# Performance work log

Hardware: AMD Instinct MI355X
Metric: run time of the kernel (lower is better)

## Reference

```python
import jax, jax.numpy as jnp
import numpy as np

NUM_CLASSES = 100000   # vocab (input_dim of the layer)
DIM = 256              # embedding dim (output_dim of the layer)
BATCH = 256
NUM_TRUE = 1024        # hardcoded num_true in call()
NUM_SAMPLED = 16384    # hardcoded num_sampled in call()
LOG_RANGE = float(np.log(NUM_CLASSES + 1.0))


def _sample_log_uniform_unique(rng, n, range_max):
    # Mimics tf log_uniform_candidate_sampler with unique=True: rejection-sample
    # from P(c) ~ log((c+2)/(c+1)) until n unique ids are collected.
    seen = {}
    log_range = np.log(range_max + 1.0)
    while len(seen) < n:
        u = rng.uniform(0.0, log_range, size=2 * n)
        ids = np.minimum(np.floor(np.exp(u) - 1.0).astype(np.int64), range_max - 1)
        for v in ids.tolist():
            if len(seen) >= n:
                break
            seen[v] = None
    return np.fromiter(seen.keys(), dtype=np.int64, count=n)


def setup_inputs() -> dict:
    key = jax.random.key(0)
    k1, k2, k3, k4 = jax.random.split(key, 4)
    inputs = jax.random.normal(k1, (BATCH, DIM), jnp.float32)
    # Original inits w/b to zeros; use small random values for a non-degenerate baseline.
    w = jax.random.normal(k2, (NUM_CLASSES, DIM), jnp.float32) * 0.02
    b = jax.random.normal(k3, (NUM_CLASSES,), jnp.float32) * 0.02
    labels = jax.random.randint(k4, (BATCH, NUM_TRUE), 0, NUM_CLASSES, dtype=jnp.int32)
    rng = np.random.default_rng(0)
    sampled = jnp.asarray(_sample_log_uniform_unique(rng, NUM_SAMPLED, NUM_CLASSES), jnp.int32)
    return {"inputs": inputs, "w": w, "b": b, "labels": labels, "sampled": sampled}


def _log_uniform_prob(ids):
    idf = ids.astype(jnp.float32)
    return jnp.log((idf + 2.0) / (idf + 1.0)) / LOG_RANGE


def _expected_count(ids):
    # P(id appears among NUM_SAMPLED unique candidates) = 1 - (1-p)^NUM_SAMPLED
    p = _log_uniform_prob(ids)
    return -jnp.expm1(NUM_SAMPLED * jnp.log1p(-p))


def _sigmoid_xent(logits, target):
    # numerically stable sigmoid cross-entropy, target is a scalar label value
    return jnp.maximum(logits, 0.0) - logits * target + jnp.log1p(jnp.exp(-jnp.abs(logits)))


def reference(inputs, w, b, labels, sampled):
    # true logits: per-example dot with each true class row  [B, T]
    true_w = w[labels]                                    # [B, T, D] gather
    true_logits = jnp.einsum('bd,btd->bt', inputs, true_w) + b[labels]
    true_logits = true_logits - jnp.log(_expected_count(labels))
    # sampled logits: shared candidate set  [B, S]
    sampled_logits = inputs @ w[sampled].T + b[sampled]
    sampled_logits = sampled_logits - jnp.log(_expected_count(sampled))
    # NCE targets: 1/num_true for true classes, 0 for sampled; sum over columns
    true_xent = _sigmoid_xent(true_logits, 1.0 / NUM_TRUE)
    sampled_xent = _sigmoid_xent(sampled_logits, 0.0)
    return true_xent.sum(axis=1) + sampled_xent.sum(axis=1)   # [B]
```

## Files before the change

### kernel.cpp

```cpp
#include <hip/hip_runtime.h>
#include <hip/hip_bf16.h>

#define NUM_CLASSES 100000
#define DIM 256
#define BATCH 256
#define NUM_TRUE 1024
#define NUM_SAMPLED 16384
#define LOG_RANGE 11.51293546492023f
#define INV_LOG_RANGE (1.0f / LOG_RANGE)

typedef __bf16 bf16x8 __attribute__((ext_vector_type(8)));
typedef float  f32x4  __attribute__((ext_vector_type(4)));

static __device__ __forceinline__ unsigned short f2bf(float f) {
    unsigned int u = __float_as_uint(f);
    unsigned int lsb = (u >> 16) & 1u;
    u += 0x7fffu + lsb;
    return (unsigned short)(u >> 16);
}

static __device__ __forceinline__ float neg_log_ec(int id) {
    float idf = (float)id;
    float p = logf((idf + 2.0f) / (idf + 1.0f)) * INV_LOG_RANGE;
    float ec = -expm1f((float)NUM_SAMPLED * log1pf(-p));
    return -logf(ec);
}

static __device__ __forceinline__ float dot4(float4 a, float4 b) {
    return fmaf(a.x, b.x, fmaf(a.y, b.y, fmaf(a.z, b.z, a.w * b.w)));
}

__global__ __launch_bounds__(256) void comb_kernel(const float* __restrict__ bias,
                                                   float* __restrict__ comb) {
    int c = blockIdx.x * 256 + threadIdx.x;
    if (c < NUM_CLASSES) comb[c] = bias[c] + neg_log_ec(c);
}

__global__ __launch_bounds__(256) void true_kernel(const float* __restrict__ inputs,
                                                   const float* __restrict__ w,
                                                   const float* __restrict__ comb,
                                                   const int* __restrict__ labels,
                                                   float* __restrict__ truep) {
    __shared__ __align__(16) float ins[DIM];
    __shared__ float wsum[4];
    const int tid = threadIdx.x;
    const int b = blockIdx.y;
    ins[tid] = inputs[b * DIM + tid];
    __syncthreads();

    const int lane = tid & 63;
    const int wv   = tid >> 6;
    const int sub  = lane >> 4;
    const int part = lane & 15;
    const float4* ir = (const float4*)ins;
    const float4 in0 = ir[part], in1 = ir[16 + part], in2 = ir[32 + part], in3 = ir[48 + part];

    const int* lab = labels + b * NUM_TRUE + blockIdx.x * 128 + wv * 32;

    float4 buf[2][4];
    float  cb[2];
    #pragma unroll
    for (int s = 0; s < 2; ++s) {
        int l = lab[s * 4 + sub];
        const float4* wr = (const float4*)(w + (size_t)l * DIM);
        buf[s][0] = wr[part];      buf[s][1] = wr[16 + part];
        buf[s][2] = wr[32 + part]; buf[s][3] = wr[48 + part];
        cb[s] = comb[l];
    }

    float acc = 0.0f;
    #pragma unroll
    for (int i = 0; i < 8; ++i) {
        const int cur = i & 1;
        float4 w0 = buf[cur][0], w1 = buf[cur][1], w2 = buf[cur][2], w3 = buf[cur][3];
        float cl = cb[cur];
        if (i < 6) {
            int l = lab[(i + 2) * 4 + sub];
            const float4* wr = (const float4*)(w + (size_t)l * DIM);
            buf[cur][0] = wr[part];      buf[cur][1] = wr[16 + part];
            buf[cur][2] = wr[32 + part]; buf[cur][3] = wr[48 + part];
            cb[cur] = comb[l];
        }
        float d = dot4(w0, in0) + dot4(w1, in1) + dot4(w2, in2) + dot4(w3, in3);
        d += __shfl_xor(d, 1); d += __shfl_xor(d, 2);
        d += __shfl_xor(d, 4); d += __shfl_xor(d, 8);
        float logit = d + cl;
        float v = fmaxf(logit, 0.0f) - logit * (1.0f / (float)NUM_TRUE)
                + __logf(1.0f + __expf(-fabsf(logit)));
        acc += (part == 0) ? v : 0.0f;
    }
    acc += __shfl_xor(acc, 16); acc += __shfl_xor(acc, 32);
    if (lane == 0) wsum[wv] = acc;
    __syncthreads();
    if (tid == 0) truep[b * 8 + blockIdx.x] = wsum[0] + wsum[1] + wsum[2] + wsum[3];
}

#define LWS 264
__global__ __launch_bounds__(256) void sampled_kernel(const float* __restrict__ w,
                                                      const float* __restrict__ comb,
                                                      const int* __restrict__ sampled,
                                                      const float* __restrict__ inputs,
                                                      float* __restrict__ partial) {
    __shared__ unsigned short lw[64][LWS];
    __shared__ unsigned short li[64][LWS];
    __shared__ float cs[64];
    __shared__ float bacc[BATCH];

    const int tid = threadIdx.x;
    const int s0 = blockIdx.x * 64;
    bacc[tid] = 0.0f;

    const int inner = tid & 15;
    const int r16   = tid >> 4;

    #pragma unroll
    for (int rb = 0; rb < 4; ++rb) {
        const int r = rb * 16 + r16;
        const int id = sampled[s0 + r];
        const float* src = w + (size_t)id * DIM;
        #pragma unroll
        for (int j = 0; j < 4; ++j) {
            float4 v = *(const float4*)(src + j * 64 + inner * 4);
            ushort4 pk;
            pk.x = f2bf(v.x); pk.y = f2bf(v.y); pk.z = f2bf(v.z); pk.w = f2bf(v.w);
            *(ushort4*)(&lw[r][j * 64 + inner * 4]) = pk;
        }
    }
    if (tid < 64) cs[tid] = comb[sampled[s0 + tid]];

    const int lane = tid & 63;
    const int wv   = tid >> 6;
    const int m    = lane & 15;
    const int quad = lane >> 4;
    const int wy   = wv & 1;
    const int wx   = wv >> 1;

    for (int chunk = 0; chunk < 4; ++chunk) {
        __syncthreads();
        #pragma unroll
        for (int rb = 0; rb < 4; ++rb) {
            const int r = rb * 16 + r16;
            const float* src = inputs + (size_t)(chunk * 64 + r) * DIM;
            #pragma unroll
            for (int j = 0; j < 4; ++j) {
                float4 v = *(const float4*)(src + j * 64 + inner * 4);
                ushort4 pk;
                pk.x = f2bf(v.x); pk.y = f2bf(v.y); pk.z = f2bf(v.z); pk.w = f2bf(v.w);
                *(ushort4*)(&li[r][j * 64 + inner * 4]) = pk;
            }
        }
        __syncthreads();

        f32x4 acc00 = {0,0,0,0}, acc01 = {0,0,0,0}, acc10 = {0,0,0,0}, acc11 = {0,0,0,0};
        const unsigned short* pa0 = &lw[wy * 32 + m][quad * 8];
        const unsigned short* pa1 = &lw[wy * 32 + 16 + m][quad * 8];
        const unsigned short* pb0 = &li[wx * 32 + m][quad * 8];
        const unsigned short* pb1 = &li[wx * 32 + 16 + m][quad * 8];
        #pragma unroll
        for (int kk = 0; kk < 8; ++kk) {
            bf16x8 a0 = *(const bf16x8*)(pa0 + kk * 32);
            bf16x8 a1 = *(const bf16x8*)(pa1 + kk * 32);
            bf16x8 b0 = *(const bf16x8*)(pb0 + kk * 32);
            bf16x8 b1 = *(const bf16x8*)(pb1 + kk * 32);
            acc00 = __builtin_amdgcn_mfma_f32_16x16x32_bf16(a0, b0, acc00, 0, 0, 0);
            acc01 = __builtin_amdgcn_mfma_f32_16x16x32_bf16(a0, b1, acc01, 0, 0, 0);
            acc10 = __builtin_amdgcn_mfma_f32_16x16x32_bf16(a1, b0, acc10, 0, 0, 0);
            acc11 = __builtin_amdgcn_mfma_f32_16x16x32_bf16(a1, b1, acc11, 0, 0, 0);
        }

        float ps0 = 0.0f, ps1 = 0.0f;
        #pragma unroll
        for (int r = 0; r < 4; ++r) {
            {
                float c = cs[wy * 32 + quad * 4 + r];
                float l0 = acc00[r] + c;
                ps0 += fmaxf(l0, 0.0f) + __logf(1.0f + __expf(-fabsf(l0)));
                float l1 = acc01[r] + c;
                ps1 += fmaxf(l1, 0.0f) + __logf(1.0f + __expf(-fabsf(l1)));
            }
            {
                float c = cs[wy * 32 + 16 + quad * 4 + r];
                float l0 = acc10[r] + c;
                ps0 += fmaxf(l0, 0.0f) + __logf(1.0f + __expf(-fabsf(l0)));
                float l1 = acc11[r] + c;
                ps1 += fmaxf(l1, 0.0f) + __logf(1.0f + __expf(-fabsf(l1)));
            }
        }
        ps0 += __shfl_xor(ps0, 16); ps0 += __shfl_xor(ps0, 32);
        ps1 += __shfl_xor(ps1, 16); ps1 += __shfl_xor(ps1, 32);
        if (quad == 0) {
            atomicAdd(&bacc[chunk * 64 + wx * 32 + m], ps0);
            atomicAdd(&bacc[chunk * 64 + wx * 32 + 16 + m], ps1);
        }
    }
    __syncthreads();
    partial[tid * 256 + blockIdx.x] = bacc[tid];
}

__global__ __launch_bounds__(256) void reduce_kernel(const float* __restrict__ partial,
                                                     const float* __restrict__ truep,
                                                     float* __restrict__ out) {
    __shared__ float wsum[4];
    const int b = blockIdx.x;
    const int tid = threadIdx.x;
    float v = partial[b * 256 + tid];
    if (tid < 8) v += truep[b * 8 + tid];
    v += __shfl_xor(v, 1);  v += __shfl_xor(v, 2);  v += __shfl_xor(v, 4);
    v += __shfl_xor(v, 8);  v += __shfl_xor(v, 16); v += __shfl_xor(v, 32);
    if ((tid & 63) == 0) wsum[tid >> 6] = v;
    __syncthreads();
    if (tid == 0) out[b] = wsum[0] + wsum[1] + wsum[2] + wsum[3];
}

extern "C" void kernel_launch(void* const* d_in, const int* in_sizes, int n_in,
                              void* d_out, int out_size, void* d_ws, size_t ws_size,
                              hipStream_t stream) {
    const float* inputs  = (const float*)d_in[0];
    const float* w       = (const float*)d_in[1];
    const float* bias    = (const float*)d_in[2];
    const int*   labels  = (const int*)d_in[3];
    const int*   sampled = (const int*)d_in[4];
    float* out = (float*)d_out;

    float* comb    = (float*)d_ws;
    float* truep   = (float*)((char*)d_ws + 409600);
    float* partial = (float*)((char*)d_ws + 417792);

    comb_kernel<<<(NUM_CLASSES + 255) / 256, 256, 0, stream>>>(bias, comb);
    true_kernel<<<dim3(8, 256), 256, 0, stream>>>(inputs, w, comb, labels, truep);
    sampled_kernel<<<256, 256, 0, stream>>>(w, comb, sampled, inputs, partial);
    reduce_kernel<<<BATCH, 256, 0, stream>>>(partial, truep, out);
}
```

Before: 189.6 us.

## Fuse true and sampled kernels into one launch with pre-converted bf16 inputs

Merges the true-logit and sampled-logit kernels into one grid, where the first 512 blocks handle 32 sampled classes each and the remaining 2048 blocks handle the true labels. The input matrix is converted to bf16 once in the comb kernel, so sampled blocks read B fragments directly from global memory instead of restaging them through shared memory per chunk. The intent is to remove a launch, let the two workloads overlap on the GPU, and increase sampled-side parallelism. In exchange, inputs are re-read from global/L2 by every sampled block and the reduce kernel reads twice as many partials.

```diff
diff --git a/kernel.cpp b/kernel.cpp
--- a/kernel.cpp
+++ b/kernel.cpp
@@ -9,6 +9,9 @@
 #define LOG_RANGE 11.51293546492023f
 #define INV_LOG_RANGE (1.0f / LOG_RANGE)
 
+#define SBLOCKS 512
+#define TBLOCKS 2048
+
 typedef __bf16 bf16x8 __attribute__((ext_vector_type(8)));
 typedef float  f32x4  __attribute__((ext_vector_type(4)));
 
@@ -31,170 +34,142 @@
 }
 
 __global__ __launch_bounds__(256) void comb_kernel(const float* __restrict__ bias,
-                                                   float* __restrict__ comb) {
+                                                   const float* __restrict__ inputs,
+                                                   float* __restrict__ comb,
+                                                   unsigned short* __restrict__ inbf) {
     int c = blockIdx.x * 256 + threadIdx.x;
     if (c < NUM_CLASSES) comb[c] = bias[c] + neg_log_ec(c);
-}
-
-__global__ __launch_bounds__(256) void true_kernel(const float* __restrict__ inputs,
-                                                   const float* __restrict__ w,
-                                                   const float* __restrict__ comb,
-                                                   const int* __restrict__ labels,
-                                                   float* __restrict__ truep) {
+    if (c < BATCH * DIM) inbf[c] = f2bf(inputs[c]);
+}
+
+__global__ __launch_bounds__(256) void fused_kernel(const float* __restrict__ inputs,
+                                                    const float* __restrict__ w,
+                                                    const float* __restrict__ comb,
+                                                    const int* __restrict__ labels,
+                                                    const int* __restrict__ sampled,
+                                                    const unsigned short* __restrict__ inbf,
+                                                    float* __restrict__ truep,
+                                                    float* __restrict__ partial) {
+    __shared__ unsigned short lw[32][264];
+    __shared__ float cs[32];
+    __shared__ float bacc[BATCH];
     __shared__ __align__(16) float ins[DIM];
     __shared__ float wsum[4];
+
     const int tid = threadIdx.x;
-    const int b = blockIdx.y;
-    ins[tid] = inputs[b * DIM + tid];
-    __syncthreads();
-
-    const int lane = tid & 63;
-    const int wv   = tid >> 6;
-    const int sub  = lane >> 4;
-    const int part = lane & 15;
-    const float4* ir = (const float4*)ins;
-    const float4 in0 = ir[part], in1 = ir[16 + part], in2 = ir[32 + part], in3 = ir[48 + part];
-
-    const int* lab = labels + b * NUM_TRUE + blockIdx.x * 128 + wv * 32;
-
-    float4 buf[2][4];
-    float  cb[2];
-    #pragma unroll
-    for (int s = 0; s < 2; ++s) {
-        int l = lab[s * 4 + sub];
-        const float4* wr = (const float4*)(w + (size_t)l * DIM);
-        buf[s][0] = wr[part];      buf[s][1] = wr[16 + part];
-        buf[s][2] = wr[32 + part]; buf[s][3] = wr[48 + part];
-        cb[s] = comb[l];
-    }
-
-    float acc = 0.0f;
-    #pragma unroll
-    for (int i = 0; i < 8; ++i) {
-        const int cur = i & 1;
-        float4 w0 = buf[cur][0], w1 = buf[cur][1], w2 = buf[cur][2], w3 = buf[cur][3];
-        float cl = cb[cur];
-        if (i < 6) {
-            int l = lab[(i + 2) * 4 + sub];
-            const float4* wr = (const float4*)(w + (size_t)l * DIM);
-            buf[cur][0] = wr[part];      buf[cur][1] = wr[16 + part];
-            buf[cur][2] = wr[32 + part]; buf[cur][3] = wr[48 + part];
-            cb[cur] = comb[l];
-        }
-        float d = dot4(w0, in0) + dot4(w1, in1) + dot4(w2, in2) + dot4(w3, in3);
-        d += __shfl_xor(d, 1); d += __shfl_xor(d, 2);
-        d += __shfl_xor(d, 4); d += __shfl_xor(d, 8);
-        float logit = d + cl;
-        float v = fmaxf(logit, 0.0f) - logit * (1.0f / (float)NUM_TRUE)
-                + __logf(1.0f + __expf(-fabsf(logit)));
-        acc += (part == 0) ? v : 0.0f;
-    }
-    acc += __shfl_xor(acc, 16); acc += __shfl_xor(acc, 32);
-    if (lane == 0) wsum[wv] = acc;
-    __syncthreads();
-    if (tid == 0) truep[b * 8 + blockIdx.x] = wsum[0] + wsum[1] + wsum[2] + wsum[3];
-}
-
-#define LWS 264
-__global__ __launch_bounds__(256) void sampled_kernel(const float* __restrict__ w,
-                                                      const float* __restrict__ comb,
-                                                      const int* __restrict__ sampled,
-                                                      const float* __restrict__ inputs,
-                                                      float* __restrict__ partial) {
-    __shared__ unsigned short lw[64][LWS];
-    __shared__ unsigned short li[64][LWS];
-    __shared__ float cs[64];
-    __shared__ float bacc[BATCH];
-
-    const int tid = threadIdx.x;
-    const int s0 = blockIdx.x * 64;
-    bacc[tid] = 0.0f;
-
-    const int inner = tid & 15;
-    const int r16   = tid >> 4;
-
-    #pragma unroll
-    for (int rb = 0; rb < 4; ++rb) {
-        const int r = rb * 16 + r16;
-        const int id = sampled[s0 + r];
-        const float* src = w + (size_t)id * DIM;
-        #pragma unroll
-        for (int j = 0; j < 4; ++j) {
-            float4 v = *(const float4*)(src + j * 64 + inner * 4);
-            ushort4 pk;
-            pk.x = f2bf(v.x); pk.y = f2bf(v.y); pk.z = f2bf(v.z); pk.w = f2bf(v.w);
-            *(ushort4*)(&lw[r][j * 64 + inner * 4]) = pk;
-        }
-    }
-    if (tid < 64) cs[tid] = comb[sampled[s0 + tid]];
-
-    const int lane = tid & 63;
-    const int wv   = tid >> 6;
-    const int m    = lane & 15;
-    const int quad = lane >> 4;
-    const int wy   = wv & 1;
-    const int wx   = wv >> 1;
-
-    for (int chunk = 0; chunk < 4; ++chunk) {
-        __syncthreads();
-        #pragma unroll
-        for (int rb = 0; rb < 4; ++rb) {
+
+    if (blockIdx.x < SBLOCKS) {
+        const int sblk = blockIdx.x;
+        const int s0 = sblk * 32;
+        bacc[tid] = 0.0f;
+
+        const int inner = tid & 15;
+        const int r16   = tid >> 4;
+        #pragma unroll
+        for (int rb = 0; rb < 2; ++rb) {
             const int r = rb * 16 + r16;
-            const float* src = inputs + (size_t)(chunk * 64 + r) * DIM;
+            const int id = sampled[s0 + r];
+            const float* src = w + (size_t)id * DIM;
             #pragma unroll
             for (int j = 0; j < 4; ++j) {
                 float4 v = *(const float4*)(src + j * 64 + inner * 4);
                 ushort4 pk;
                 pk.x = f2bf(v.x); pk.y = f2bf(v.y); pk.z = f2bf(v.z); pk.w = f2bf(v.w);
-                *(ushort4*)(&li[r][j * 64 + inner * 4]) = pk;
+                *(ushort4*)(&lw[r][j * 64 + inner * 4]) = pk;
             }
         }
-        __syncthreads();
-
-        f32x4 acc00 = {0,0,0,0}, acc01 = {0,0,0,0}, acc10 = {0,0,0,0}, acc11 = {0,0,0,0};
-        const unsigned short* pa0 = &lw[wy * 32 + m][quad * 8];
-        const unsigned short* pa1 = &lw[wy * 32 + 16 + m][quad * 8];
-        const unsigned short* pb0 = &li[wx * 32 + m][quad * 8];
-        const unsigned short* pb1 = &li[wx * 32 + 16 + m][quad * 8];
-        #pragma unroll
-        for (int kk = 0; kk < 8; ++kk) {
-            bf16x8 a0 = *(const bf16x8*)(pa0 + kk * 32);
-            bf16x8 a1 = *(const bf16x8*)(pa1 + kk * 32);
-            bf16x8 b0 = *(const bf16x8*)(pb0 + kk * 32);
-            bf16x8 b1 = *(const bf16x8*)(pb1 + kk * 32);
-            acc00 = __builtin_amdgcn_mfma_f32_16x16x32_bf16(a0, b0, acc00, 0, 0, 0);
-            acc01 = __builtin_amdgcn_mfma_f32_16x16x32_bf16(a0, b1, acc01, 0, 0, 0);
-            acc10 = __builtin_amdgcn_mfma_f32_16x16x32_bf16(a1, b0, acc10, 0, 0, 0);
-            acc11 = __builtin_amdgcn_mfma_f32_16x16x32_bf16(a1, b1, acc11, 0, 0, 0);
-        }
-
-        float ps0 = 0.0f, ps1 = 0.0f;
-        #pragma unroll
-        for (int r = 0; r < 4; ++r) {
-            {
-                float c = cs[wy * 32 + quad * 4 + r];
-                float l0 = acc00[r] + c;
-                ps0 += fmaxf(l0, 0.0f) + __logf(1.0f + __expf(-fabsf(l0)));
-                float l1 = acc01[r] + c;
-                ps1 += fmaxf(l1, 0.0f) + __logf(1.0f + __expf(-fabsf(l1)));
+        if (tid < 32) cs[tid] = comb[sampled[s0 + tid]];
+        __syncthreads();
+
+        const int lane = tid & 63;
+        const int wv   = tid >> 6;
+        const int m    = lane & 15;
+        const int quad = lane >> 4;
+        const int shalf = (wv >> 1) * 16;
+        const int bhalf = (wv & 1) * 128;
+
+        bf16x8 af[8];
+        #pragma unroll
+        for (int kk = 0; kk < 8; ++kk)
+            af[kk] = *(const bf16x8*)(&lw[shalf + m][kk * 32 + quad * 8]);
+
+        #pragma unroll
+        for (int t = 0; t < 8; ++t) {
+            const int brow = bhalf + t * 16 + m;
+            const unsigned short* bp = inbf + brow * DIM;
+            bf16x8 bf[8];
+            #pragma unroll
+            for (int kk = 0; kk < 8; ++kk)
+                bf[kk] = *(const bf16x8*)(bp + kk * 32 + quad * 8);
+            f32x4 acc = {0, 0, 0, 0};
+            #pragma unroll
+            for (int kk = 0; kk < 8; ++kk)
+                acc = __builtin_amdgcn_mfma_f32_16x16x32_bf16(af[kk], bf[kk], acc, 0, 0, 0);
+            float ps = 0.0f;
+            #pragma unroll
+            for (int r = 0; r < 4; ++r) {
+                float c = cs[shalf + quad * 4 + r];
+                float l = acc[r] + c;
+                ps += fmaxf(l, 0.0f) + __logf(1.0f + __expf(-fabsf(l)));
             }
-            {
-                float c = cs[wy * 32 + 16 + quad * 4 + r];
-                float l0 = acc10[r] + c;
-                ps0 += fmaxf(l0, 0.0f) + __logf(1.0f + __expf(-fabsf(l0)));
-                float l1 = acc11[r] + c;
-                ps1 += fmaxf(l1, 0.0f) + __logf(1.0f + __expf(-fabsf(l1)));
+            ps += __shfl_xor(ps, 16); ps += __shfl_xor(ps, 32);
+            if (quad == 0) atomicAdd(&bacc[bhalf + t * 16 + m], ps);
+        }
+        __syncthreads();
+        partial[tid * SBLOCKS + sblk] = bacc[tid];
+    } else {
+        const int bid  = blockIdx.x - SBLOCKS;
+        const int b    = bid >> 3;
+        const int chnk = bid & 7;
+        ins[tid] = inputs[b * DIM + tid];
+        __syncthreads();
+
+        const int lane = tid & 63;
+        const int wv   = tid >> 6;
+        const int sub  = lane >> 4;
+        const int part = lane & 15;
+        const float4* ir = (const float4*)ins;
+        const float4 in0 = ir[part], in1 = ir[16 + part], in2 = ir[32 + part], in3 = ir[48 + part];
+
+        const int* lab = labels + b * NUM_TRUE + chnk * 128 + wv * 32;
+
+        float4 buf[2][4];
+        float  cb[2];
+        #pragma unroll
+        for (int s = 0; s < 2; ++s) {
+            int l = lab[s * 4 + sub];
+            const float4* wr = (const float4*)(w + (size_t)l * DIM);
+            buf[s][0] = wr[part];      buf[s][1] = wr[16 + part];
+            buf[s][2] = wr[32 + part]; buf[s][3] = wr[48 + part];
+            cb[s] = comb[l];
+        }
+
+        float acc = 0.0f;
+        #pragma unroll
+        for (int i = 0; i < 8; ++i) {
+            const int cur = i & 1;
+            float4 w0 = buf[cur][0], w1 = buf[cur][1], w2 = buf[cur][2], w3 = buf[cur][3];
+            float cl = cb[cur];
+            if (i < 6) {
+                int l = lab[(i + 2) * 4 + sub];
+                const float4* wr = (const float4*)(w + (size_t)l * DIM);
+                buf[cur][0] = wr[part];      buf[cur][1] = wr[16 + part];
+                buf[cur][2] = wr[32 + part]; buf[cur][3] = wr[48 + part];
+                cb[cur] = comb[l];
             }
-        }
-        ps0 += __shfl_xor(ps0, 16); ps0 += __shfl_xor(ps0, 32);
-        ps1 += __shfl_xor(ps1, 16); ps1 += __shfl_xor(ps1, 32);
-        if (quad == 0) {
-            atomicAdd(&bacc[chunk * 64 + wx * 32 + m], ps0);
-            atomicAdd(&bacc[chunk * 64 + wx * 32 + 16 + m], ps1);
-        }
+            float d = dot4(w0, in0) + dot4(w1, in1) + dot4(w2, in2) + dot4(w3, in3);
+            d += __shfl_xor(d, 1); d += __shfl_xor(d, 2);
+            d += __shfl_xor(d, 4); d += __shfl_xor(d, 8);
+            float logit = d + cl;
+            float v = fmaxf(logit, 0.0f) - logit * (1.0f / (float)NUM_TRUE)
+                    + __logf(1.0f + __expf(-fabsf(logit)));
+            acc += (part == 0) ? v : 0.0f;
+        }
+        acc += __shfl_xor(acc, 16); acc += __shfl_xor(acc, 32);
+        if (lane == 0) wsum[wv] = acc;
+        __syncthreads();
+        if (tid == 0) truep[b * 8 + chnk] = wsum[0] + wsum[1] + wsum[2] + wsum[3];
     }
-    __syncthreads();
-    partial[tid * 256 + blockIdx.x] = bacc[tid];
 }
 
 __global__ __launch_bounds__(256) void reduce_kernel(const float* __restrict__ partial,
@@ -203,7 +178,7 @@
     __shared__ float wsum[4];
     const int b = blockIdx.x;
     const int tid = threadIdx.x;
-    float v = partial[b * 256 + tid];
+    float v = partial[b * SBLOCKS + tid] + partial[b * SBLOCKS + 256 + tid];
     if (tid < 8) v += truep[b * 8 + tid];
     v += __shfl_xor(v, 1);  v += __shfl_xor(v, 2);  v += __shfl_xor(v, 4);
     v += __shfl_xor(v, 8);  v += __shfl_xor(v, 16); v += __shfl_xor(v, 32);
@@ -222,12 +197,13 @@
     const int*   sampled = (const int*)d_in[4];
     float* out = (float*)d_out;
 
-    float* comb    = (float*)d_ws;
-    float* truep   = (float*)((char*)d_ws + 409600);
-    float* partial = (float*)((char*)d_ws + 417792);
-
-    comb_kernel<<<(NUM_CLASSES + 255) / 256, 256, 0, stream>>>(bias, comb);
-    true_kernel<<<dim3(8, 256), 256, 0, stream>>>(inputs, w, comb, labels, truep);
-    sampled_kernel<<<256, 256, 0, stream>>>(w, comb, sampled, inputs, partial);
+    float*          comb    = (float*)d_ws;
+    unsigned short* inbf    = (unsigned short*)((char*)d_ws + 409600);
+    float*          truep   = (float*)((char*)d_ws + 540672);
+    float*          partial = (float*)((char*)d_ws + 548864);
+
+    comb_kernel<<<(NUM_CLASSES + 255) / 256, 256, 0, stream>>>(bias, inputs, comb, inbf);
+    fused_kernel<<<SBLOCKS + TBLOCKS, 256, 0, stream>>>(inputs, w, comb, labels,
+                                                        sampled, inbf, truep, partial);
     reduce_kernel<<<BATCH, 256, 0, stream>>>(partial, truep, out);
 }
```

After: 179.0 us. -5.6%, faster.
